# Kernel tuning notes

Hardware: AMD Instinct MI355X
Metric: run time of the kernel (lower is better)

Reference implementation:

```python
import jax, jax.numpy as jnp
import numpy as np


def setup_inputs() -> dict:
    key = jax.random.key(0)
    kq, ks, kr, kx, ky = jax.random.split(key, 5)
    B, C, H, W, K = 2, 64, 128, 256, 32
    Q = jax.random.normal(kq, (B, C, H, W), dtype=jnp.float32)
    S = jax.random.normal(ks, (B, C, H, W), dtype=jnp.float32)
    R = jax.random.normal(kr, (B, C, H, W), dtype=jnp.float32)
    Pos_x = jax.random.randint(kx, (H * W, K), 0, H, dtype=jnp.int64 if jax.config.jax_enable_x64 else jnp.int32)
    Pos_y = jax.random.randint(ky, (H * W, K), 0, W, dtype=jnp.int64 if jax.config.jax_enable_x64 else jnp.int32)
    return {"Q": Q, "S": S, "R": R, "Pos_x": Pos_x, "Pos_y": Pos_y}


def reference(Q, S, R, Pos_x, Pos_y):
    B, C, H, W = Q.shape
    N = H * W
    px = Pos_x.reshape(-1)  # [N*K]
    py = Pos_y.reshape(-1)
    K = px.shape[0] // N
    # Gather keys/values at candidate positions: [B, C, N*K] -> [B, C, N, K]
    Key = S[:, :, px, py].reshape(B, C, N, K)
    Value = R[:, :, px, py].reshape(B, C, N, K)
    # Queries: [B, N, C]
    Qf = Q.reshape(B, C, N).transpose(0, 2, 1)
    # Per-pixel scores over K candidates (NO 1/sqrt(d) scaling, as in original)
    score = jnp.einsum('bnc,bcnk->bnk', Qf, Key)
    attn = jax.nn.softmax(score, axis=-1)
    # Attention-weighted sum of values: [B, N, C]
    out = jnp.einsum('bnk,bcnk->bnc', attn, Value)
    return out.reshape(B, H, W, C).transpose(0, 3, 1, 2)
```

## Files before the change

### kernel.cpp

```cpp
#include <hip/hip_runtime.h>
#include <hip/hip_fp16.h>

constexpr int B = 2, C = 64, H = 128, W = 256, N = H * W, K = 32;

typedef _Float16 hf2 __attribute__((ext_vector_type(2)));

template <int CTRL>
__device__ __forceinline__ float dppf(float x) {
    int i = __builtin_bit_cast(int, x);
    int r = __builtin_amdgcn_update_dpp(i, i, CTRL, 0xF, 0xF, false);
    return __builtin_bit_cast(float, r);
}

__device__ __forceinline__ unsigned sel4(const uint4& v, int g) {
    return g == 0 ? v.x : g == 1 ? v.y : g == 2 ? v.z : v.w;
}
__device__ __forceinline__ unsigned sel4(const ushort4& v, int g) {
    return g == 0 ? v.x : g == 1 ? v.y : g == 2 ? v.z : v.w;
}

__global__ __launch_bounds__(256) void fepam_prep(
    const float* __restrict__ Q, const float* __restrict__ S,
    const float* __restrict__ R,
    const int* __restrict__ Px, const int* __restrict__ Py,
    __half* __restrict__ Qt, __half* __restrict__ St, __half* __restrict__ Rt,
    unsigned short* __restrict__ Idx) {
    const int n0 = blockIdx.x * 64;
    const int b  = blockIdx.y;
    const int z  = blockIdx.z;

    if (z == 3) {
        if (b) return;
#pragma unroll
        for (int t = 0; t < 8; ++t) {
            const int e  = threadIdx.x + 256 * t;
            const int nl = e >> 5, k = e & 31;
            const int n  = n0 + nl;
            const int idx = Px[(size_t)n * K + k] * W + Py[(size_t)n * K + k];
            Idx[(size_t)n * K + (k & 7) * 4 + (k >> 3)] = (unsigned short)idx;
        }
        return;
    }

    __shared__ float tile[C][65];
    const float* src = (z == 0 ? S : (z == 1 ? R : Q)) + (size_t)b * C * N;
    __half2* d2 = (__half2*)((z == 0 ? St : (z == 1 ? Rt : Qt)) +
                             (size_t)b * N * C);
    {
        const int j = threadIdx.x & 63, c0 = threadIdx.x >> 6;
        const float* s = src + n0 + j;
#pragma unroll
        for (int r = 0; r < 16; ++r) {
            int c = c0 + r * 4;
            tile[c][j] = s[(size_t)c * N];
        }
    }
    __syncthreads();
    {
        const int c2 = threadIdx.x & 31, j0 = threadIdx.x >> 5;
#pragma unroll
        for (int r = 0; r < 8; ++r) {
            int j = j0 + 8 * r;
            d2[(size_t)(n0 + j) * 32 + c2] =
                __floats2half2_rn(tile[2 * c2][j], tile[2 * c2 + 1][j]);
        }
    }
}

__global__ __launch_bounds__(256, 6) void fepam_scores(
    const __half* __restrict__ Qt, const unsigned short* __restrict__ Idx,
    const __half* __restrict__ St, unsigned* __restrict__ AI) {
    const int tid  = threadIdx.x;
    const int lane = tid & 63;
    const int wave = tid >> 6;
    const int bx   = blockIdx.x;
    const int b    = bx & 1;
    const int n0   = (bx >> 1) * 32 + wave * 8;

    const int c_oct = lane & 7;
    const int k_loc = lane >> 3;

    const __half* Qtb = Qt + (size_t)b * N * C;
    const __half* Stb = St + (size_t)b * N * C;
    unsigned* AIb = AI + (size_t)b * N * K;

    auto ldi = [&](int p) {
        return *(const ushort4*)(Idx + (size_t)(n0 + p) * K + k_loc * 4);
    };
    auto ldq = [&](int p) {
        return *(const float4*)(Qtb + (size_t)(n0 + p) * C + c_oct * 8);
    };
    auto ldk = [&](const ushort4& iv, int g) {
        return *(const float4*)(Stb + ((size_t)sel4(iv, g) << 6) + c_oct * 8);
    };

    ushort4 iv_c = ldi(0), iv_n = ldi(1);
    float4  q_c  = ldq(0), q_n  = ldq(1);
    float4  k_c[4];
#pragma unroll
    for (int g = 0; g < 4; ++g) k_c[g] = ldk(iv_c, g);

#pragma unroll
    for (int p = 0; p < 8; ++p) {
        float4 k_n[4];
        if (p < 7) {
#pragma unroll
            for (int g = 0; g < 4; ++g) k_n[g] = ldk(iv_n, g);
        }
        ushort4 iv_2;
        float4  q_2;
        if (p < 6) { iv_2 = ldi(p + 2); q_2 = ldq(p + 2); }

        float s[4];
#pragma unroll
        for (int g = 0; g < 4; ++g) {
            const hf2* k2 = (const hf2*)&k_c[g];
            const hf2* q2 = (const hf2*)&q_c;
            float acc = 0.f;
#pragma unroll
            for (int u = 0; u < 4; ++u)
                acc = __builtin_amdgcn_fdot2(k2[u], q2[u], acc, false);
            s[g] = acc;
        }
#pragma unroll
        for (int g = 0; g < 4; ++g) {
            s[g] += dppf<0xB1>(s[g]);
            s[g] += dppf<0x4E>(s[g]);
            s[g] += dppf<0x141>(s[g]);
        }
        float m = fmaxf(fmaxf(s[0], s[1]), fmaxf(s[2], s[3]));
        m = fmaxf(m, dppf<0x128>(m));
        m = fmaxf(m, __shfl_xor(m, 16));
        m = fmaxf(m, __shfl_xor(m, 32));
        float e0 = __expf(s[0] - m), e1 = __expf(s[1] - m);
        float e2 = __expf(s[2] - m), e3 = __expf(s[3] - m);
        float l = (e0 + e1) + (e2 + e3);
        l += dppf<0x128>(l);
        l += __shfl_xor(l, 16);
        l += __shfl_xor(l, 32);
        const float inv = 1.0f / l;

        if (c_oct == 0) {
            uint4 wv;
            wv.x = ((unsigned)iv_c.x << 16) |
                   __half_as_ushort(__float2half_rn(e0 * inv));
            wv.y = ((unsigned)iv_c.y << 16) |
                   __half_as_ushort(__float2half_rn(e1 * inv));
            wv.z = ((unsigned)iv_c.z << 16) |
                   __half_as_ushort(__float2half_rn(e2 * inv));
            wv.w = ((unsigned)iv_c.w << 16) |
                   __half_as_ushort(__float2half_rn(e3 * inv));
            *(uint4*)(AIb + (size_t)(n0 + p) * K + k_loc * 4) = wv;
        }

#pragma unroll
        for (int g = 0; g < 4; ++g) k_c[g] = k_n[g];
        iv_c = iv_n; q_c = q_n;
        iv_n = iv_2; q_n = q_2;
    }
}

__global__ __launch_bounds__(256, 6) void fepam_values(
    const unsigned* __restrict__ AI, const __half* __restrict__ Rt,
    float* __restrict__ Out) {
    __shared__ __align__(16) float ot[32][66];

    const int tid  = threadIdx.x;
    const int lane = tid & 63;
    const int wave = tid >> 6;
    const int bx   = blockIdx.x;
    const int b    = bx & 1;
    const int n0t  = (bx >> 1) * 32;
    const int n0   = n0t + wave * 8;

    const int c_oct = lane & 7;
    const int k_loc = lane >> 3;
    const bool hi8  = (lane & 8)  != 0;
    const bool hi16 = (lane & 16) != 0;
    const bool hi32 = (lane & 32) != 0;

    const __half* Rtb = Rt + (size_t)b * N * C;
    const unsigned* AIb = AI + (size_t)b * N * K;

    auto ldw = [&](int p) {
        return *(const uint4*)(AIb + (size_t)(n0 + p) * K + k_loc * 4);
    };
    auto ldv = [&](const uint4& wv, int g) {
        return *(const float4*)(Rtb + ((size_t)(sel4(wv, g) >> 16) << 6) +
                                c_oct * 8);
    };

    uint4  w_c = ldw(0), w_n = ldw(1);
    float4 v_c[4];
#pragma unroll
    for (int g = 0; g < 4; ++g) v_c[g] = ldv(w_c, g);

#pragma unroll
    for (int p = 0; p < 8; ++p) {
        float4 v_n[4];
        if (p < 7) {
#pragma unroll
            for (int g = 0; g < 4; ++g) v_n[g] = ldv(w_n, g);
        }
        uint4 w_2;
        if (p < 6) w_2 = ldw(p + 2);

        const float a[4] = {
            __half2float(__ushort_as_half((unsigned short)(w_c.x & 0xffffu))),
            __half2float(__ushort_as_half((unsigned short)(w_c.y & 0xffffu))),
            __half2float(__ushort_as_half((unsigned short)(w_c.z & 0xffffu))),
            __half2float(__ushort_as_half((unsigned short)(w_c.w & 0xffffu)))};
        float acc[8] = {0, 0, 0, 0, 0, 0, 0, 0};
#pragma unroll
        for (int g = 0; g < 4; ++g) {
            const __half2* v2 = (const __half2*)&v_c[g];
#pragma unroll
            for (int u = 0; u < 4; ++u) {
                const float2 vf = __half22float2(v2[u]);
                acc[2 * u]     = fmaf(a[g], vf.x, acc[2 * u]);
                acc[2 * u + 1] = fmaf(a[g], vf.y, acc[2 * u + 1]);
            }
        }

        float r4[4];
#pragma unroll
        for (int i = 0; i < 4; ++i) {
            const float send = hi8 ? acc[i] : acc[4 + i];
            const float recv = dppf<0x128>(send);
            r4[i] = (hi8 ? acc[4 + i] : acc[i]) + recv;
        }
        float r2[2];
#pragma unroll
        for (int i = 0; i < 2; ++i) {
            const float send = hi16 ? r4[i] : r4[2 + i];
            const float recv = __shfl_xor(send, 16);
            r2[i] = (hi16 ? r4[2 + i] : r4[i]) + recv;
        }
        {
            const float send = hi32 ? r2[0] : r2[1];
            const float recv = __shfl_xor(send, 32);
            const float r1   = (hi32 ? r2[1] : r2[0]) + recv;
            const int c = c_oct * 8 + (hi8 ? 4 : 0) + (hi16 ? 2 : 0) + (hi32 ? 1 : 0);
            ot[wave * 8 + p][c] = r1;
        }

#pragma unroll
        for (int g = 0; g < 4; ++g) v_c[g] = v_n[g];
        w_c = w_n;
        w_n = w_2;
    }
    __syncthreads();

    {
        const int j = tid & 31, c0 = tid >> 5;
        float* od = Out + (size_t)b * C * N + n0t + j;
#pragma unroll
        for (int r = 0; r < 8; ++r) {
            int c = c0 + r * 8;
            od[(size_t)c * N] = ot[j][c];
        }
    }
}

extern "C" void kernel_launch(void* const* d_in, const int* in_sizes, int n_in,
                              void* d_out, int out_size, void* d_ws, size_t ws_size,
                              hipStream_t stream) {
    const float* Q  = (const float*)d_in[0];
    const float* S  = (const float*)d_in[1];
    const float* R  = (const float*)d_in[2];
    const int*   Px = (const int*)d_in[3];
    const int*   Py = (const int*)d_in[4];
    float* Out = (float*)d_out;

    __half* St = (__half*)d_ws;
    __half* Rt = St + (size_t)B * N * C;
    __half* Qt = Rt + (size_t)B * N * C;
    unsigned short* Idx = (unsigned short*)(Qt + (size_t)B * N * C);
    unsigned* AI = (unsigned*)(Idx + (size_t)N * K);

    dim3 pgrid(N / 64, B, 4);
    fepam_prep<<<pgrid, 256, 0, stream>>>(Q, S, R, Px, Py, Qt, St, Rt, Idx);

    dim3 ggrid(N / 32 * B);
    fepam_scores<<<ggrid, 256, 0, stream>>>(Qt, Idx, St, AI);
    fepam_values<<<ggrid, 256, 0, stream>>>(AI, Rt, Out);
}
```

Baseline: 136.0 us.

## Split transposed fp16 feature maps into two channel planes for gathers

The prep kernel now writes S, R and Q in fp16 as two separate 32-channel planes per batch instead of one interleaved 64-channel row per pixel. The scores and values kernels make two passes, one per plane, gathering 64-byte rows instead of 128-byte rows, and accumulate partial dot products across the passes. The aim is a smaller per-plane working set for the random gathers so more of it stays in cache. In exchange the index reads and loop overhead are doubled, gathers are narrower, more registers hold the partial scores, and the values reduction leaves half the lanes idle on the final step.

```diff
diff --git a/kernel.cpp b/kernel.cpp
--- a/kernel.cpp
+++ b/kernel.cpp
@@ -44,8 +44,7 @@
 
     __shared__ float tile[C][65];
     const float* src = (z == 0 ? S : (z == 1 ? R : Q)) + (size_t)b * C * N;
-    __half2* d2 = (__half2*)((z == 0 ? St : (z == 1 ? Rt : Qt)) +
-                             (size_t)b * N * C);
+    __half2* d2 = (__half2*)(z == 0 ? St : (z == 1 ? Rt : Qt));
     {
         const int j = threadIdx.x & 63, c0 = threadIdx.x >> 6;
         const float* s = src + n0 + j;
@@ -58,10 +57,11 @@
     __syncthreads();
     {
         const int c2 = threadIdx.x & 31, j0 = threadIdx.x >> 5;
+        const int plane = c2 >> 4, c2l = c2 & 15;
 #pragma unroll
         for (int r = 0; r < 8; ++r) {
             int j = j0 + 8 * r;
-            d2[(size_t)(n0 + j) * 32 + c2] =
+            d2[((size_t)(2 * b + plane) * N + (n0 + j)) * 16 + c2l] =
                 __floats2half2_rn(tile[2 * c2][j], tile[2 * c2 + 1][j]);
         }
     }
@@ -80,60 +80,85 @@
     const int c_oct = lane & 7;
     const int k_loc = lane >> 3;
 
-    const __half* Qtb = Qt + (size_t)b * N * C;
-    const __half* Stb = St + (size_t)b * N * C;
     unsigned* AIb = AI + (size_t)b * N * K;
 
     auto ldi = [&](int p) {
         return *(const ushort4*)(Idx + (size_t)(n0 + p) * K + k_loc * 4);
     };
-    auto ldq = [&](int p) {
-        return *(const float4*)(Qtb + (size_t)(n0 + p) * C + c_oct * 8);
-    };
-    auto ldk = [&](const ushort4& iv, int g) {
-        return *(const float4*)(Stb + ((size_t)sel4(iv, g) << 6) + c_oct * 8);
-    };
-
-    ushort4 iv_c = ldi(0), iv_n = ldi(1);
-    float4  q_c  = ldq(0), q_n  = ldq(1);
-    float4  k_c[4];
-#pragma unroll
-    for (int g = 0; g < 4; ++g) k_c[g] = ldk(iv_c, g);
+
+    float s[8][4];
+#pragma unroll
+    for (int p = 0; p < 8; ++p)
+#pragma unroll
+        for (int g = 0; g < 4; ++g) s[p][g] = 0.f;
+    ushort4 ivs[8];
+
+#pragma unroll
+    for (int P = 0; P < 2; ++P) {
+        const __half* Kp = St + (size_t)(2 * b + P) * N * 32;
+        const __half* Qp = Qt + (size_t)(2 * b + P) * N * 32;
+
+        auto ldq = [&](int p) {
+            return *(const float2*)(Qp + (size_t)(n0 + p) * 32 + c_oct * 4);
+        };
+        auto ldk = [&](const ushort4& iv, int g) {
+            return *(const float2*)(Kp + (size_t)sel4(iv, g) * 32 + c_oct * 4);
+        };
+
+        ushort4 iv_c = ldi(0), iv_n = ldi(1);
+        float2  q_c  = ldq(0), q_n  = ldq(1);
+        float2  k_c[4];
+#pragma unroll
+        for (int g = 0; g < 4; ++g) k_c[g] = ldk(iv_c, g);
+
+#pragma unroll
+        for (int p = 0; p < 8; ++p) {
+            float2 k_n[4];
+            if (p < 7) {
+#pragma unroll
+                for (int g = 0; g < 4; ++g) k_n[g] = ldk(iv_n, g);
+            }
+            ushort4 iv_2;
+            float2  q_2;
+            if (p < 6) { iv_2 = ldi(p + 2); q_2 = ldq(p + 2); }
+
+            if (P == 0) ivs[p] = iv_c;
+
+            const hf2* q2 = (const hf2*)&q_c;
+#pragma unroll
+            for (int g = 0; g < 4; ++g) {
+                const hf2* k2 = (const hf2*)&k_c[g];
+                float acc = s[p][g];
+#pragma unroll
+                for (int u = 0; u < 2; ++u)
+                    acc = __builtin_amdgcn_fdot2(k2[u], q2[u], acc, false);
+                s[p][g] = acc;
+            }
+
+#pragma unroll
+            for (int g = 0; g < 4; ++g) k_c[g] = k_n[g];
+            iv_c = iv_n; q_c = q_n;
+            iv_n = iv_2; q_n = q_2;
+        }
+    }
 
 #pragma unroll
     for (int p = 0; p < 8; ++p) {
-        float4 k_n[4];
-        if (p < 7) {
-#pragma unroll
-            for (int g = 0; g < 4; ++g) k_n[g] = ldk(iv_n, g);
-        }
-        ushort4 iv_2;
-        float4  q_2;
-        if (p < 6) { iv_2 = ldi(p + 2); q_2 = ldq(p + 2); }
-
-        float s[4];
+        float t[4];
 #pragma unroll
         for (int g = 0; g < 4; ++g) {
-            const hf2* k2 = (const hf2*)&k_c[g];
-            const hf2* q2 = (const hf2*)&q_c;
-            float acc = 0.f;
-#pragma unroll
-            for (int u = 0; u < 4; ++u)
-                acc = __builtin_amdgcn_fdot2(k2[u], q2[u], acc, false);
-            s[g] = acc;
-        }
-#pragma unroll
-        for (int g = 0; g < 4; ++g) {
-            s[g] += dppf<0xB1>(s[g]);
-            s[g] += dppf<0x4E>(s[g]);
-            s[g] += dppf<0x141>(s[g]);
-        }
-        float m = fmaxf(fmaxf(s[0], s[1]), fmaxf(s[2], s[3]));
+            float v = s[p][g];
+            v += dppf<0xB1>(v);
+            v += dppf<0x4E>(v);
+            v += dppf<0x141>(v);
+            t[g] = v;
+        }
+        float m = fmaxf(fmaxf(t[0], t[1]), fmaxf(t[2], t[3]));
         m = fmaxf(m, dppf<0x128>(m));
         m = fmaxf(m, __shfl_xor(m, 16));
         m = fmaxf(m, __shfl_xor(m, 32));
-        float e0 = __expf(s[0] - m), e1 = __expf(s[1] - m);
-        float e2 = __expf(s[2] - m), e3 = __expf(s[3] - m);
+        float e0 = __expf(t[0] - m), e1 = __expf(t[1] - m);
+        float e2 = __expf(t[2] - m), e3 = __expf(t[3] - m);
         float l = (e0 + e1) + (e2 + e3);
         l += dppf<0x128>(l);
         l += __shfl_xor(l, 16);
@@ -141,22 +166,18 @@
         const float inv = 1.0f / l;
 
         if (c_oct == 0) {
+            const ushort4 iv = ivs[p];
             uint4 wv;
-            wv.x = ((unsigned)iv_c.x << 16) |
+            wv.x = ((unsigned)iv.x << 16) |
                    __half_as_ushort(__float2half_rn(e0 * inv));
-            wv.y = ((unsigned)iv_c.y << 16) |
+            wv.y = ((unsigned)iv.y << 16) |
                    __half_as_ushort(__float2half_rn(e1 * inv));
-            wv.z = ((unsigned)iv_c.z << 16) |
+            wv.z = ((unsigned)iv.z << 16) |
                    __half_as_ushort(__float2half_rn(e2 * inv));
-            wv.w = ((unsigned)iv_c.w << 16) |
+            wv.w = ((unsigned)iv.w << 16) |
                    __half_as_ushort(__float2half_rn(e3 * inv));
             *(uint4*)(AIb + (size_t)(n0 + p) * K + k_loc * 4) = wv;
         }
-
-#pragma unroll
-        for (int g = 0; g < 4; ++g) k_c[g] = k_n[g];
-        iv_c = iv_n; q_c = q_n;
-        iv_n = iv_2; q_n = q_2;
     }
 }
 
@@ -179,75 +200,78 @@
     const bool hi16 = (lane & 16) != 0;
     const bool hi32 = (lane & 32) != 0;
 
-    const __half* Rtb = Rt + (size_t)b * N * C;
     const unsigned* AIb = AI + (size_t)b * N * K;
 
     auto ldw = [&](int p) {
         return *(const uint4*)(AIb + (size_t)(n0 + p) * K + k_loc * 4);
     };
-    auto ldv = [&](const uint4& wv, int g) {
-        return *(const float4*)(Rtb + ((size_t)(sel4(wv, g) >> 16) << 6) +
-                                c_oct * 8);
-    };
-
-    uint4  w_c = ldw(0), w_n = ldw(1);
-    float4 v_c[4];
-#pragma unroll
-    for (int g = 0; g < 4; ++g) v_c[g] = ldv(w_c, g);
-
-#pragma unroll
-    for (int p = 0; p < 8; ++p) {
-        float4 v_n[4];
-        if (p < 7) {
-#pragma unroll
-            for (int g = 0; g < 4; ++g) v_n[g] = ldv(w_n, g);
-        }
-        uint4 w_2;
-        if (p < 6) w_2 = ldw(p + 2);
-
-        const float a[4] = {
-            __half2float(__ushort_as_half((unsigned short)(w_c.x & 0xffffu))),
-            __half2float(__ushort_as_half((unsigned short)(w_c.y & 0xffffu))),
-            __half2float(__ushort_as_half((unsigned short)(w_c.z & 0xffffu))),
-            __half2float(__ushort_as_half((unsigned short)(w_c.w & 0xffffu)))};
-        float acc[8] = {0, 0, 0, 0, 0, 0, 0, 0};
-#pragma unroll
-        for (int g = 0; g < 4; ++g) {
-            const __half2* v2 = (const __half2*)&v_c[g];
-#pragma unroll
-            for (int u = 0; u < 4; ++u) {
-                const float2 vf = __half22float2(v2[u]);
-                acc[2 * u]     = fmaf(a[g], vf.x, acc[2 * u]);
-                acc[2 * u + 1] = fmaf(a[g], vf.y, acc[2 * u + 1]);
-            }
-        }
-
-        float r4[4];
-#pragma unroll
-        for (int i = 0; i < 4; ++i) {
-            const float send = hi8 ? acc[i] : acc[4 + i];
-            const float recv = dppf<0x128>(send);
-            r4[i] = (hi8 ? acc[4 + i] : acc[i]) + recv;
-        }
-        float r2[2];
-#pragma unroll
-        for (int i = 0; i < 2; ++i) {
-            const float send = hi16 ? r4[i] : r4[2 + i];
-            const float recv = __shfl_xor(send, 16);
-            r2[i] = (hi16 ? r4[2 + i] : r4[i]) + recv;
-        }
-        {
-            const float send = hi32 ? r2[0] : r2[1];
-            const float recv = __shfl_xor(send, 32);
-            const float r1   = (hi32 ? r2[1] : r2[0]) + recv;
-            const int c = c_oct * 8 + (hi8 ? 4 : 0) + (hi16 ? 2 : 0) + (hi32 ? 1 : 0);
-            ot[wave * 8 + p][c] = r1;
-        }
-
-#pragma unroll
-        for (int g = 0; g < 4; ++g) v_c[g] = v_n[g];
-        w_c = w_n;
-        w_n = w_2;
+
+#pragma unroll
+    for (int P = 0; P < 2; ++P) {
+        const __half* Vp = Rt + (size_t)(2 * b + P) * N * 32;
+
+        auto ldv = [&](const uint4& wv, int g) {
+            return *(const float2*)(Vp + (size_t)(sel4(wv, g) >> 16) * 32 +
+                                    c_oct * 4);
+        };
+
+        uint4  w_c = ldw(0), w_n = ldw(1);
+        float2 v_c[4];
+#pragma unroll
+        for (int g = 0; g < 4; ++g) v_c[g] = ldv(w_c, g);
+
+#pragma unroll
+        for (int p = 0; p < 8; ++p) {
+            float2 v_n[4];
+            if (p < 7) {
+#pragma unroll
+                for (int g = 0; g < 4; ++g) v_n[g] = ldv(w_n, g);
+            }
+            uint4 w_2;
+            if (p < 6) w_2 = ldw(p + 2);
+
+            const float a[4] = {
+                __half2float(__ushort_as_half((unsigned short)(w_c.x & 0xffffu))),
+                __half2float(__ushort_as_half((unsigned short)(w_c.y & 0xffffu))),
+                __half2float(__ushort_as_half((unsigned short)(w_c.z & 0xffffu))),
+                __half2float(__ushort_as_half((unsigned short)(w_c.w & 0xffffu)))};
+            float acc[4] = {0.f, 0.f, 0.f, 0.f};
+#pragma unroll
+            for (int g = 0; g < 4; ++g) {
+                const __half2* v2 = (const __half2*)&v_c[g];
+                const float2 f0 = __half22float2(v2[0]);
+                const float2 f1 = __half22float2(v2[1]);
+                acc[0] = fmaf(a[g], f0.x, acc[0]);
+                acc[1] = fmaf(a[g], f0.y, acc[1]);
+                acc[2] = fmaf(a[g], f1.x, acc[2]);
+                acc[3] = fmaf(a[g], f1.y, acc[3]);
+            }
+
+            float r2[2];
+#pragma unroll
+            for (int i = 0; i < 2; ++i) {
+                const float send = hi8 ? acc[i] : acc[2 + i];
+                const float recv = dppf<0x128>(send);
+                r2[i] = (hi8 ? acc[2 + i] : acc[i]) + recv;
+            }
+            float r1;
+            {
+                const float send = hi16 ? r2[0] : r2[1];
+                const float recv = __shfl_xor(send, 16);
+                r1 = (hi16 ? r2[1] : r2[0]) + recv;
+            }
+            r1 += __shfl_xor(r1, 32);
+            if (!hi32) {
+                const int c =
+                    P * 32 + c_oct * 4 + (hi8 ? 2 : 0) + (hi16 ? 1 : 0);
+                ot[wave * 8 + p][c] = r1;
+            }
+
+#pragma unroll
+            for (int g = 0; g < 4; ++g) v_c[g] = v_n[g];
+            w_c = w_n;
+            w_n = w_2;
+        }
     }
     __syncthreads();
 
```

Result: slower. 377.5 us (+177.5%).
